# Kernel tuning notes

Hardware: AMD Instinct MI355X
Metric: run time of the kernel (lower is better)

## Reference

```python
import jax, jax.numpy as jnp
import numpy as np

SAMPLE_RATE = 16000
HUM_FREQ = 60
Q_FACTOR = 30.0
BATCH = 128
SAMPLES = 160000


def _notch_sos(freq, Q, fs):
    # scipy.signal.iirnotch closed form (gb = 1/sqrt(2) -> beta = tan(bw/2))
    w0 = 2.0 * np.pi * freq / fs
    beta = np.tan(w0 / (2.0 * Q))
    gain = 1.0 / (1.0 + beta)
    b0 = gain
    b1 = -2.0 * gain * np.cos(w0)
    b2 = gain
    a1 = -2.0 * gain * np.cos(w0)
    a2 = 2.0 * gain - 1.0
    # tf2sos of a 2nd-order TF: single section [b0,b1,b2,a0=1,a1,a2]
    return [b0, b1, b2, 1.0, a1, a2]


def _build_sos():
    rows = []
    for f in (HUM_FREQ, HUM_FREQ * 2, HUM_FREQ * 3):
        if f < SAMPLE_RATE / 2:
            rows.append(_notch_sos(f, Q_FACTOR, SAMPLE_RATE))
    return np.asarray(rows, dtype=np.float32)  # [3, 6]


def setup_inputs() -> dict:
    key = jax.random.key(0)
    audio = jax.random.normal(key, (BATCH, SAMPLES), dtype=jnp.float32)
    sos = jnp.asarray(_build_sos())  # [n_sections, 6], a0 == 1
    return {"audio": audio, "sos": sos}


def _sosfilt(sos, x):
    """Cascaded biquad IIR (direct form II transposed), matching scipy.sosfilt.
    sos: [n_sections, 6] with a0 == 1.  x: [B, T].  Returns [B, T].
    """
    n_sections = sos.shape[0]
    B = x.shape[0]

    def step(z, xt):  # z: [n_sections, 2, B], xt: [B]
        y = xt
        new_z = []
        for s in range(n_sections):
            b0, b1, b2 = sos[s, 0], sos[s, 1], sos[s, 2]
            a1, a2 = sos[s, 4], sos[s, 5]
            out = b0 * y + z[s, 0]
            z0 = b1 * y - a1 * out + z[s, 1]
            z1 = b2 * y - a2 * out
            new_z.append(jnp.stack([z0, z1]))
            y = out
        return jnp.stack(new_z), y

    z_init = jnp.zeros((n_sections, 2, B), dtype=x.dtype)
    _, ys = jax.lax.scan(step, z_init, x.T)  # ys: [T, B]
    return ys.T


def reference(audio, sos):
    squeeze = audio.ndim == 1
    a = audio[None, :] if squeeze else audio
    y = _sosfilt(sos, a)
    return y[0] if squeeze else y
```

## Files before the change

kernel.cpp:

```cpp
#include <hip/hip_runtime.h>

#define B_ROWS 128
#define T_SAMP 160000
#define NSEC 3
#define LCH 20
#define NRND 5
#define RST 21
#define SUPW 1280
#define NSUP 125
#define WPB 4
#define NMAT_P 6
#define NMAT_Q 7

struct Coefs {
  float b0[NSEC], b1[NSEC], b2[NSEC], a1[NSEC], a2[NSEC];
};

__device__ __forceinline__ void load_coefs(const float* __restrict__ sos, Coefs& c) {
#pragma unroll
  for (int s = 0; s < NSEC; ++s) {
    c.b0[s] = sos[s * 6 + 0];
    c.b1[s] = sos[s * 6 + 1];
    c.b2[s] = sos[s * 6 + 2];
    c.a1[s] = sos[s * 6 + 4];
    c.a2[s] = sos[s * 6 + 5];
  }
}

__device__ __forceinline__ float df2t_step(const Coefs& c, float z[6], float x) {
  float y = x;
#pragma unroll
  for (int s = 0; s < NSEC; ++s) {
    float out = fmaf(c.b0[s], y, z[2 * s]);
    float t0  = fmaf(c.b1[s], y, z[2 * s + 1]);
    z[2 * s]     = fmaf(-c.a1[s], out, t0);
    float t1  = c.b2[s] * y;
    z[2 * s + 1] = fmaf(-c.a2[s], out, t1);
    y = out;
  }
  return y;
}

__device__ __forceinline__ float dmm6(float a, float b, int i, int j) {
  float s = 0.f;
#pragma unroll
  for (int k = 0; k < 6; ++k)
    s = fmaf(__shfl(a, i * 6 + k), __shfl(b, k * 6 + j), s);
  return s;
}

__global__ __launch_bounds__(64) void setup_kernel(const float* __restrict__ sos,
                                                   float* __restrict__ mats) {
  const int lane = threadIdx.x;
  const int e = (lane < 36) ? lane : 0;
  const int i = e / 6, j = e % 6;
  Coefs cf; load_coefs(sos, cf);

  float A[36];
#pragma unroll
  for (int jc = 0; jc < 6; ++jc) {
    float z[6] = {0.f, 0.f, 0.f, 0.f, 0.f, 0.f};
    z[jc] = 1.0f;
    df2t_step(cf, z, 0.0f);
#pragma unroll
    for (int ic = 0; ic < 6; ++ic) A[ic * 6 + jc] = z[ic];
  }
  float a = A[e];

  float a2  = dmm6(a, a, i, j);
  float a4  = dmm6(a2, a2, i, j);
  float a8  = dmm6(a4, a4, i, j);
  float a16 = dmm6(a8, a8, i, j);
  float p[NMAT_P];
  p[0] = dmm6(a16, a4, i, j);
#pragma unroll
  for (int k = 1; k < NMAT_P; ++k) p[k] = dmm6(p[k - 1], p[k - 1], i, j);
  float q[NMAT_Q];
  q[0] = dmm6(p[5], p[5], i, j);
#pragma unroll
  for (int k = 1; k < NMAT_Q; ++k) q[k] = dmm6(q[k - 1], q[k - 1], i, j);

  if (lane < 36) {
#pragma unroll
    for (int k = 0; k < NMAT_P; ++k) mats[k * 36 + lane] = p[k];
#pragma unroll
    for (int k = 0; k < NMAT_Q; ++k) mats[(NMAT_P + k) * 36 + lane] = q[k];
  }
}

__global__ __launch_bounds__(256) void pass1_kernel(const float* __restrict__ x,
                                                    const float* __restrict__ sos,
                                                    const float* __restrict__ mats,
                                                    float* __restrict__ Fsup) {
  __shared__ float Bsh[WPB * 64 * RST + NMAT_P * 36];
  float* Pm = Bsh + WPB * 64 * RST;
  const int tid = threadIdx.x;
  const int w = tid >> 6, lane = tid & 63;
  for (int t = tid; t < NMAT_P * 36; t += 256) Pm[t] = mats[t];
  __syncthreads();

  const int S = blockIdx.x * WPB + w;
  const int r = S / NSUP, s = S - r * NSUP;
  Coefs cf; load_coefs(sos, cf);

  const float* src = x + (size_t)r * T_SAMP + (size_t)s * SUPW;
  float* lds = Bsh + w * 64 * RST;
#pragma unroll
  for (int i2 = 0; i2 < NRND; ++i2) {
    int q = i2 * 64 + lane, k = q / NRND, m = q - k * NRND;
    float4 v = *reinterpret_cast<const float4*>(src + 4 * q);
    int lo = k * RST + m * 4;
    lds[lo + 0] = v.x; lds[lo + 1] = v.y; lds[lo + 2] = v.z; lds[lo + 3] = v.w;
  }
  __syncthreads();

  float f[6] = {0.f, 0.f, 0.f, 0.f, 0.f, 0.f};
#pragma unroll
  for (int jj = 0; jj < LCH; ++jj) df2t_step(cf, f, lds[lane * RST + jj]);

#pragma unroll
  for (int k = 0; k < 6; ++k) {
    float t[6];
#pragma unroll
    for (int e = 0; e < 6; ++e) t[e] = __shfl_up(f[e], 1 << k);
    if (lane >= (1 << k)) {
      const float* P = Pm + k * 36;
      float nf[6];
#pragma unroll
      for (int e = 0; e < 6; ++e) {
        float acc = f[e];
#pragma unroll
        for (int kk = 0; kk < 6; ++kk) acc = fmaf(P[e * 6 + kk], t[kk], acc);
        nf[e] = acc;
      }
#pragma unroll
      for (int e = 0; e < 6; ++e) f[e] = nf[e];
    }
  }
  if (lane == 63) {
    float* fo = Fsup + (size_t)S * 6;
#pragma unroll
    for (int e = 0; e < 6; ++e) fo[e] = f[e];
  }
}

__global__ __launch_bounds__(64) void middle_scan(const float* __restrict__ Fsup,
                                                  const float* __restrict__ mats,
                                                  float* __restrict__ zsup) {
  __shared__ float Qm[NMAT_Q * 36];
  const int r = blockIdx.x, lane = threadIdx.x;
  for (int t = lane; t < NMAT_Q * 36; t += 64) Qm[t] = mats[NMAT_P * 36 + t];
  __syncthreads();

  const float* frow = Fsup + (size_t)r * NSUP * 6;
  float fc[2][6];
#pragma unroll
  for (int jj = 0; jj < 2; ++jj) {
    int c = 2 * lane + jj;
#pragma unroll
    for (int e = 0; e < 6; ++e) fc[jj][e] = (c < NSUP) ? frow[c * 6 + e] : 0.f;
  }
  float s[6] = {0.f, 0.f, 0.f, 0.f, 0.f, 0.f};
#pragma unroll
  for (int jj = 0; jj < 2; ++jj) {
    float ns[6];
#pragma unroll
    for (int e = 0; e < 6; ++e) {
      float acc = fc[jj][e];
#pragma unroll
      for (int kk = 0; kk < 6; ++kk) acc = fmaf(Qm[e * 6 + kk], s[kk], acc);
      ns[e] = acc;
    }
#pragma unroll
    for (int e = 0; e < 6; ++e) s[e] = ns[e];
  }
#pragma unroll
  for (int k = 0; k < 6; ++k) {
    float t[6];
#pragma unroll
    for (int e = 0; e < 6; ++e) t[e] = __shfl_up(s[e], 1 << k);
    if (lane >= (1 << k)) {
      const float* Q = Qm + (k + 1) * 36;
      float ns[6];
#pragma unroll
      for (int e = 0; e < 6; ++e) {
        float acc = s[e];
#pragma unroll
        for (int kk = 0; kk < 6; ++kk) acc = fmaf(Q[e * 6 + kk], t[kk], acc);
        ns[e] = acc;
      }
#pragma unroll
      for (int e = 0; e < 6; ++e) s[e] = ns[e];
    }
  }
  float z[6];
#pragma unroll
  for (int e = 0; e < 6; ++e) {
    float t = __shfl_up(s[e], 1);
    z[e] = (lane == 0) ? 0.f : t;
  }
  float* zrow = zsup + (size_t)r * NSUP * 6;
#pragma unroll
  for (int jj = 0; jj < 2; ++jj) {
    int c = 2 * lane + jj;
    if (c < NSUP) {
#pragma unroll
      for (int e = 0; e < 6; ++e) zrow[c * 6 + e] = z[e];
    }
    float nz[6];
#pragma unroll
    for (int e = 0; e < 6; ++e) {
      float acc = fc[jj][e];
#pragma unroll
      for (int kk = 0; kk < 6; ++kk) acc = fmaf(Qm[e * 6 + kk], z[kk], acc);
      nz[e] = acc;
    }
#pragma unroll
    for (int e = 0; e < 6; ++e) z[e] = nz[e];
  }
}

__global__ __launch_bounds__(256) void pass2_kernel(const float* __restrict__ x,
                                                    const float* __restrict__ sos,
                                                    const float* __restrict__ mats,
                                                    const float* __restrict__ zsup,
                                                    float* __restrict__ y) {
  __shared__ float Bsh[WPB * 64 * RST + NMAT_P * 36];
  float* Pm = Bsh + WPB * 64 * RST;
  const int tid = threadIdx.x;
  const int w = tid >> 6, lane = tid & 63;
  for (int t = tid; t < NMAT_P * 36; t += 256) Pm[t] = mats[t];
  __syncthreads();

  const int S = blockIdx.x * WPB + w;
  const int r = S / NSUP, s = S - r * NSUP;
  Coefs cf; load_coefs(sos, cf);

  const float* src = x + (size_t)r * T_SAMP + (size_t)s * SUPW;
  float* dst = y + (size_t)r * T_SAMP + (size_t)s * SUPW;
  float* lds = Bsh + w * 64 * RST;
  int lofs[NRND];
#pragma unroll
  for (int i2 = 0; i2 < NRND; ++i2) {
    int q = i2 * 64 + lane, k = q / NRND, m = q - k * NRND;
    lofs[i2] = k * RST + m * 4;
    float4 v = *reinterpret_cast<const float4*>(src + 4 * q);
    lds[lofs[i2] + 0] = v.x; lds[lofs[i2] + 1] = v.y;
    lds[lofs[i2] + 2] = v.z; lds[lofs[i2] + 3] = v.w;
  }
  __syncthreads();

  float f[6] = {0.f, 0.f, 0.f, 0.f, 0.f, 0.f};
#pragma unroll
  for (int jj = 0; jj < LCH; ++jj) df2t_step(cf, f, lds[lane * RST + jj]);

  float z0[6];
  const float* zp = zsup + (size_t)S * 6;
#pragma unroll
  for (int e = 0; e < 6; ++e) z0[e] = zp[e];
  if (lane == 0) {
    float nf[6];
#pragma unroll
    for (int e = 0; e < 6; ++e) {
      float acc = f[e];
#pragma unroll
      for (int kk = 0; kk < 6; ++kk) acc = fmaf(Pm[e * 6 + kk], z0[kk], acc);
      nf[e] = acc;
    }
#pragma unroll
    for (int e = 0; e < 6; ++e) f[e] = nf[e];
  }
#pragma unroll
  for (int k = 0; k < 6; ++k) {
    float t[6];
#pragma unroll
    for (int e = 0; e < 6; ++e) t[e] = __shfl_up(f[e], 1 << k);
    if (lane >= (1 << k)) {
      const float* P = Pm + k * 36;
      float nf[6];
#pragma unroll
      for (int e = 0; e < 6; ++e) {
        float acc = f[e];
#pragma unroll
        for (int kk = 0; kk < 6; ++kk) acc = fmaf(P[e * 6 + kk], t[kk], acc);
        nf[e] = acc;
      }
#pragma unroll
      for (int e = 0; e < 6; ++e) f[e] = nf[e];
    }
  }
  float zs[6];
#pragma unroll
  for (int e = 0; e < 6; ++e) {
    float t = __shfl_up(f[e], 1);
    zs[e] = (lane == 0) ? z0[e] : t;
  }
#pragma unroll
  for (int jj = 0; jj < LCH; ++jj) {
    float out = df2t_step(cf, zs, lds[lane * RST + jj]);
    lds[lane * RST + jj] = out;
  }
  __syncthreads();
#pragma unroll
  for (int i2 = 0; i2 < NRND; ++i2) {
    float4 wv;
    wv.x = lds[lofs[i2] + 0]; wv.y = lds[lofs[i2] + 1];
    wv.z = lds[lofs[i2] + 2]; wv.w = lds[lofs[i2] + 3];
    *reinterpret_cast<float4*>(dst + 4 * (i2 * 64 + lane)) = wv;
  }
}

extern "C" void kernel_launch(void* const* d_in, const int* in_sizes, int n_in,
                              void* d_out, int out_size, void* d_ws, size_t ws_size,
                              hipStream_t stream) {
  const float* x = (const float*)d_in[0];
  const float* sos = (const float*)d_in[1];
  float* y = (float*)d_out;

  const int NS = B_ROWS * NSUP;
  float* Fsup = (float*)d_ws;
  float* zsup = Fsup + (size_t)NS * 6;
  float* mats = zsup + (size_t)NS * 6;

  hipLaunchKernelGGL(setup_kernel, dim3(1), dim3(64), 0, stream, sos, mats);
  hipLaunchKernelGGL(pass1_kernel, dim3(NS / WPB), dim3(256), 0, stream, x, sos, mats, Fsup);
  hipLaunchKernelGGL(middle_scan, dim3(B_ROWS), dim3(64), 0, stream, Fsup, mats, zsup);
  hipLaunchKernelGGL(pass2_kernel, dim3(NS / WPB), dim3(256), 0, stream, x, sos, mats, zsup, y);
}
```

Before: 71.59 us.

## Load chunks directly to registers and exploit block-triangular state transition matrices

```diff
diff --git a/kernel.cpp b/kernel.cpp
--- a/kernel.cpp
+++ b/kernel.cpp
@@ -4,7 +4,7 @@
 #define T_SAMP 160000
 #define NSEC 3
 #define LCH 20
-#define NRND 5
+#define NF4 5
 #define RST 21
 #define SUPW 1280
 #define NSUP 125
@@ -41,6 +41,22 @@
   return y;
 }
 
+__device__ __forceinline__ void tri_combine(float f[6], const float* __restrict__ P,
+                                            const float t[6]) {
+  float nf[6];
+#pragma unroll
+  for (int e = 0; e < 6; ++e) {
+    float acc = f[e];
+    const int kmax = ((e >> 1) << 1) + 2;
+#pragma unroll
+    for (int kk = 0; kk < 6; ++kk)
+      if (kk < kmax) acc = fmaf(P[e * 6 + kk], t[kk], acc);
+    nf[e] = acc;
+  }
+#pragma unroll
+  for (int e = 0; e < 6; ++e) f[e] = nf[e];
+}
+
 __device__ __forceinline__ float dmm6(float a, float b, int i, int j) {
   float s = 0.f;
 #pragma unroll
@@ -92,50 +108,35 @@
                                                     const float* __restrict__ sos,
                                                     const float* __restrict__ mats,
                                                     float* __restrict__ Fsup) {
-  __shared__ float Bsh[WPB * 64 * RST + NMAT_P * 36];
-  float* Pm = Bsh + WPB * 64 * RST;
+  __shared__ float Pm[NMAT_P * 36];
   const int tid = threadIdx.x;
   const int w = tid >> 6, lane = tid & 63;
   for (int t = tid; t < NMAT_P * 36; t += 256) Pm[t] = mats[t];
-  __syncthreads();
 
   const int S = blockIdx.x * WPB + w;
   const int r = S / NSUP, s = S - r * NSUP;
   Coefs cf; load_coefs(sos, cf);
 
-  const float* src = x + (size_t)r * T_SAMP + (size_t)s * SUPW;
-  float* lds = Bsh + w * 64 * RST;
-#pragma unroll
-  for (int i2 = 0; i2 < NRND; ++i2) {
-    int q = i2 * 64 + lane, k = q / NRND, m = q - k * NRND;
-    float4 v = *reinterpret_cast<const float4*>(src + 4 * q);
-    int lo = k * RST + m * 4;
-    lds[lo + 0] = v.x; lds[lo + 1] = v.y; lds[lo + 2] = v.z; lds[lo + 3] = v.w;
-  }
-  __syncthreads();
+  const float4* src = reinterpret_cast<const float4*>(
+      x + (size_t)r * T_SAMP + (size_t)s * SUPW + lane * LCH);
+  float4 v[NF4];
+#pragma unroll
+  for (int i = 0; i < NF4; ++i) v[i] = src[i];
 
   float f[6] = {0.f, 0.f, 0.f, 0.f, 0.f, 0.f};
 #pragma unroll
-  for (int jj = 0; jj < LCH; ++jj) df2t_step(cf, f, lds[lane * RST + jj]);
+  for (int i = 0; i < NF4; ++i) {
+    df2t_step(cf, f, v[i].x); df2t_step(cf, f, v[i].y);
+    df2t_step(cf, f, v[i].z); df2t_step(cf, f, v[i].w);
+  }
+  __syncthreads();
 
 #pragma unroll
   for (int k = 0; k < 6; ++k) {
     float t[6];
 #pragma unroll
     for (int e = 0; e < 6; ++e) t[e] = __shfl_up(f[e], 1 << k);
-    if (lane >= (1 << k)) {
-      const float* P = Pm + k * 36;
-      float nf[6];
-#pragma unroll
-      for (int e = 0; e < 6; ++e) {
-        float acc = f[e];
-#pragma unroll
-        for (int kk = 0; kk < 6; ++kk) acc = fmaf(P[e * 6 + kk], t[kk], acc);
-        nf[e] = acc;
-      }
-#pragma unroll
-      for (int e = 0; e < 6; ++e) f[e] = nf[e];
-    }
+    if (lane >= (1 << k)) tri_combine(f, Pm + k * 36, t);
   }
   if (lane == 63) {
     float* fo = Fsup + (size_t)S * 6;
@@ -179,19 +180,7 @@
     float t[6];
 #pragma unroll
     for (int e = 0; e < 6; ++e) t[e] = __shfl_up(s[e], 1 << k);
-    if (lane >= (1 << k)) {
-      const float* Q = Qm + (k + 1) * 36;
-      float ns[6];
-#pragma unroll
-      for (int e = 0; e < 6; ++e) {
-        float acc = s[e];
-#pragma unroll
-        for (int kk = 0; kk < 6; ++kk) acc = fmaf(Q[e * 6 + kk], t[kk], acc);
-        ns[e] = acc;
-      }
-#pragma unroll
-      for (int e = 0; e < 6; ++e) s[e] = ns[e];
-    }
+    if (lane >= (1 << k)) tri_combine(s, Qm + (k + 1) * 36, t);
   }
   float z[6];
 #pragma unroll
@@ -225,69 +214,42 @@
                                                     const float* __restrict__ mats,
                                                     const float* __restrict__ zsup,
                                                     float* __restrict__ y) {
-  __shared__ float Bsh[WPB * 64 * RST + NMAT_P * 36];
-  float* Pm = Bsh + WPB * 64 * RST;
+  __shared__ float Bsh[WPB * 64 * RST];
+  __shared__ float Pm[NMAT_P * 36];
   const int tid = threadIdx.x;
   const int w = tid >> 6, lane = tid & 63;
   for (int t = tid; t < NMAT_P * 36; t += 256) Pm[t] = mats[t];
-  __syncthreads();
 
   const int S = blockIdx.x * WPB + w;
   const int r = S / NSUP, s = S - r * NSUP;
   Coefs cf; load_coefs(sos, cf);
 
-  const float* src = x + (size_t)r * T_SAMP + (size_t)s * SUPW;
-  float* dst = y + (size_t)r * T_SAMP + (size_t)s * SUPW;
-  float* lds = Bsh + w * 64 * RST;
-  int lofs[NRND];
-#pragma unroll
-  for (int i2 = 0; i2 < NRND; ++i2) {
-    int q = i2 * 64 + lane, k = q / NRND, m = q - k * NRND;
-    lofs[i2] = k * RST + m * 4;
-    float4 v = *reinterpret_cast<const float4*>(src + 4 * q);
-    lds[lofs[i2] + 0] = v.x; lds[lofs[i2] + 1] = v.y;
-    lds[lofs[i2] + 2] = v.z; lds[lofs[i2] + 3] = v.w;
-  }
-  __syncthreads();
-
-  float f[6] = {0.f, 0.f, 0.f, 0.f, 0.f, 0.f};
-#pragma unroll
-  for (int jj = 0; jj < LCH; ++jj) df2t_step(cf, f, lds[lane * RST + jj]);
+  const size_t base = (size_t)r * T_SAMP + (size_t)s * SUPW;
+  const float4* src = reinterpret_cast<const float4*>(x + base + lane * LCH);
+  float4 v[NF4];
+#pragma unroll
+  for (int i = 0; i < NF4; ++i) v[i] = src[i];
 
   float z0[6];
   const float* zp = zsup + (size_t)S * 6;
 #pragma unroll
   for (int e = 0; e < 6; ++e) z0[e] = zp[e];
-  if (lane == 0) {
-    float nf[6];
-#pragma unroll
-    for (int e = 0; e < 6; ++e) {
-      float acc = f[e];
-#pragma unroll
-      for (int kk = 0; kk < 6; ++kk) acc = fmaf(Pm[e * 6 + kk], z0[kk], acc);
-      nf[e] = acc;
-    }
-#pragma unroll
-    for (int e = 0; e < 6; ++e) f[e] = nf[e];
-  }
+
+  float f[6] = {0.f, 0.f, 0.f, 0.f, 0.f, 0.f};
+#pragma unroll
+  for (int i = 0; i < NF4; ++i) {
+    df2t_step(cf, f, v[i].x); df2t_step(cf, f, v[i].y);
+    df2t_step(cf, f, v[i].z); df2t_step(cf, f, v[i].w);
+  }
+  __syncthreads();
+
+  if (lane == 0) tri_combine(f, Pm, z0);
 #pragma unroll
   for (int k = 0; k < 6; ++k) {
     float t[6];
 #pragma unroll
     for (int e = 0; e < 6; ++e) t[e] = __shfl_up(f[e], 1 << k);
-    if (lane >= (1 << k)) {
-      const float* P = Pm + k * 36;
-      float nf[6];
-#pragma unroll
-      for (int e = 0; e < 6; ++e) {
-        float acc = f[e];
-#pragma unroll
-        for (int kk = 0; kk < 6; ++kk) acc = fmaf(P[e * 6 + kk], t[kk], acc);
-        nf[e] = acc;
-      }
-#pragma unroll
-      for (int e = 0; e < 6; ++e) f[e] = nf[e];
-    }
+    if (lane >= (1 << k)) tri_combine(f, Pm + k * 36, t);
   }
   float zs[6];
 #pragma unroll
@@ -295,18 +257,25 @@
     float t = __shfl_up(f[e], 1);
     zs[e] = (lane == 0) ? z0[e] : t;
   }
-#pragma unroll
-  for (int jj = 0; jj < LCH; ++jj) {
-    float out = df2t_step(cf, zs, lds[lane * RST + jj]);
-    lds[lane * RST + jj] = out;
-  }
-  __syncthreads();
-#pragma unroll
-  for (int i2 = 0; i2 < NRND; ++i2) {
+
+  float* lds = Bsh + w * 64 * RST;
+#pragma unroll
+  for (int i = 0; i < NF4; ++i) {
+    lds[lane * RST + 4 * i + 0] = df2t_step(cf, zs, v[i].x);
+    lds[lane * RST + 4 * i + 1] = df2t_step(cf, zs, v[i].y);
+    lds[lane * RST + 4 * i + 2] = df2t_step(cf, zs, v[i].z);
+    lds[lane * RST + 4 * i + 3] = df2t_step(cf, zs, v[i].w);
+  }
+  __syncthreads();
+
+  float* dst = y + base;
+#pragma unroll
+  for (int i2 = 0; i2 < NF4; ++i2) {
+    int q = i2 * 64 + lane, k = q / NF4, m = q - k * NF4;
     float4 wv;
-    wv.x = lds[lofs[i2] + 0]; wv.y = lds[lofs[i2] + 1];
-    wv.z = lds[lofs[i2] + 2]; wv.w = lds[lofs[i2] + 3];
-    *reinterpret_cast<float4*>(dst + 4 * (i2 * 64 + lane)) = wv;
+    wv.x = lds[k * RST + m * 4 + 0]; wv.y = lds[k * RST + m * 4 + 1];
+    wv.z = lds[k * RST + m * 4 + 2]; wv.w = lds[k * RST + m * 4 + 3];
+    *reinterpret_cast<float4*>(dst + 4 * q) = wv;
   }
 }
 
```

Result: faster. 64.13 us (-10.4%).
